# Kernel tuning notes

Hardware: AMD Instinct MI355X
Metric: run time of the kernel (lower is better)

Reference implementation:

```python
import jax, jax.numpy as jnp
import numpy as np

B, L, E, H = 4, 2048, 1024, 16
HD = E // H  # head_dim = 64


def setup_inputs() -> dict:
    key = jax.random.key(0)
    ks = jax.random.split(key, 10)
    s = 1.0 / np.sqrt(E)
    return {
        "x": jax.random.normal(ks[0], (B, L, E), dtype=jnp.float32),
        "mask": jax.random.randint(ks[1], (B, L), 0, 2, dtype=jnp.int32),
        "Wq": jax.random.normal(ks[2], (E, E), dtype=jnp.float32) * s,
        "bq": jnp.zeros((E,), dtype=jnp.float32),
        "Wk": jax.random.normal(ks[3], (E, E), dtype=jnp.float32) * s,
        "bk": jnp.zeros((E,), dtype=jnp.float32),
        "Wv": jax.random.normal(ks[4], (E, E), dtype=jnp.float32) * s,
        "bv": jnp.zeros((E,), dtype=jnp.float32),
        "Wo": jax.random.normal(ks[5], (E, E), dtype=jnp.float32) * s,
        "bo": jnp.zeros((E,), dtype=jnp.float32),
    }


def _separate_heads(t):
    # Faithful to the torch code: a raw reshape (B, L, E) -> (B, H, L, HD),
    # NOT the usual (B, L, H, HD) + transpose.
    return t.reshape(B, H, L, HD)


def reference(x, mask, Wq, bq, Wk, bk, Wv, bv, Wo, bo):
    q = _separate_heads(x @ Wq.T + bq)
    k = _separate_heads(x @ Wk.T + bk)
    v = _separate_heads(x @ Wv.T + bv)
    scores = jnp.einsum('bhqd,bhkd->bhqk', q, k) / np.sqrt(HD).astype(np.float32)
    m = mask[:, None, None, :]  # (B,1,1,L) broadcast over (B,H,L,L)
    scores = jnp.where(m == 0, jnp.float32(-1e10), scores)
    attn = jax.nn.softmax(scores, axis=-1)
    out = jnp.einsum('bhqk,bhkd->bhqd', attn, v)
    out = out.transpose(0, 2, 1, 3).reshape(B, L, E)
    return out @ Wo.T + bo
```

## Files before the change

kernel.cpp:

```cpp
#include <hip/hip_runtime.h>
#include <hip/hip_bf16.h>

namespace {
constexpr int kB = 4, kL = 2048, kE = 1024, kH = 16, kHD = 64;
constexpr float kCs = 0.18033688f;
}

typedef __attribute__((ext_vector_type(8))) short bf16x8;
typedef __attribute__((ext_vector_type(4))) float f32x4;

__device__ __forceinline__ short f2bf(float f) {
  __hip_bfloat16 h = __float2bfloat16(f);
  return *reinterpret_cast<short*>(&h);
}

__device__ __forceinline__ void load_lds16(const void* g, void* l) {
  __builtin_amdgcn_global_load_lds((const __attribute__((address_space(1))) void*)g,
                                   (__attribute__((address_space(3))) void*)l, 16, 0, 0);
}
__device__ __forceinline__ void load_lds4(const void* g, void* l) {
  __builtin_amdgcn_global_load_lds((const __attribute__((address_space(1))) void*)g,
                                   (__attribute__((address_space(3))) void*)l, 4, 0, 0);
}

__global__ __launch_bounds__(256) void k_prep(const float* __restrict__ x,
                                              const float* __restrict__ w0,
                                              const float* __restrict__ w1,
                                              const float* __restrict__ w2,
                                              const float* __restrict__ w3,
                                              const int* __restrict__ mask,
                                              short* __restrict__ xb,
                                              short* __restrict__ wdst,
                                              float* __restrict__ mkf) {
  const int bx = blockIdx.x;
  const int tid = threadIdx.x;
  if (bx < 8192) {
    int i = (bx * 256 + tid) * 4;
    float4 v = *reinterpret_cast<const float4*>(x + i);
    short4 o;
    o.x = f2bf(v.x); o.y = f2bf(v.y); o.z = f2bf(v.z); o.w = f2bf(v.w);
    *reinterpret_cast<short4*>(xb + i) = o;
  } else if (bx < 12288) {
    int b2 = bx - 8192;
    int seg = b2 >> 10;
    const float* s = seg == 0 ? w0 : seg == 1 ? w1 : seg == 2 ? w2 : w3;
    int local = ((b2 & 1023) * 256 + tid) * 4;
    float4 v = *reinterpret_cast<const float4*>(s + local);
    short4 o;
    o.x = f2bf(v.x); o.y = f2bf(v.y); o.z = f2bf(v.z); o.w = f2bf(v.w);
    *reinterpret_cast<short4*>(wdst + seg * 1048576 + local) = o;
  } else {
    int i = (bx - 12288) * 256 + tid;
    mkf[i] = mask[i] != 0 ? -10.0f : -1.0e10f;
  }
}

__global__ __launch_bounds__(256) void k_trv(const short* __restrict__ Vl,
                                             short* __restrict__ Vt) {
  __shared__ unsigned T[64 * 33];
  const int t = threadIdx.x;
  const int hb = blockIdx.y;
  const int l0 = blockIdx.x * 64;
  const short* src = Vl + hb * 131072;
  short* dst = Vt + hb * 131072;
  const int d8 = (t & 7) * 8;
  const int lp = t >> 3;
  const uint4 va = *reinterpret_cast<const uint4*>(src + (l0 + 2 * lp) * 64 + d8);
  const uint4 vb = *reinterpret_cast<const uint4*>(src + (l0 + 2 * lp + 1) * 64 + d8);
  const unsigned a[4] = {va.x, va.y, va.z, va.w};
  const unsigned b[4] = {vb.x, vb.y, vb.z, vb.w};
#pragma unroll
  for (int j = 0; j < 4; ++j) {
    unsigned z0 = __builtin_amdgcn_perm(b[j], a[j], 0x05040100u);
    unsigned z1 = __builtin_amdgcn_perm(b[j], a[j], 0x07060302u);
    T[(d8 + 2 * j) * 33 + lp] = z0;
    T[(d8 + 2 * j + 1) * 33 + lp] = z1;
  }
  __syncthreads();
  const int u = (t & 7) * 4;
#pragma unroll
  for (int h2 = 0; h2 < 2; ++h2) {
    int d = (t >> 3) + h2 * 32;
    uint4 r;
    r.x = T[d * 33 + u];     r.y = T[d * 33 + u + 1];
    r.z = T[d * 33 + u + 2]; r.w = T[d * 33 + u + 3];
    *reinterpret_cast<uint4*>(dst + d * 2048 + l0 + u * 2) = r;
  }
}

struct GemmCore256 {
  f32x4 acc[4][4];
  int tid, w, lane, quad, m16, wm, wn;
  __device__ __forceinline__ void run(const short* __restrict__ A,
                                      const short* __restrict__ W,
                                      int bm0, int bn0, short* S) {
    tid = threadIdx.x;
    w = tid >> 6; lane = tid & 63; quad = lane >> 4; m16 = lane & 15;
    wm = (w >> 1) * 64; wn = (w & 1) * 64;
#pragma unroll
    for (int i = 0; i < 4; ++i)
#pragma unroll
      for (int j = 0; j < 4; ++j) acc[i][j] = (f32x4){0, 0, 0, 0};

    const int srow = tid >> 3;
    const int sunit = (tid & 7) ^ (srow & 7);
    const short* Ag = A + (bm0 + srow) * 1024 + sunit * 8;
    const short* Wg = W + (bn0 + srow) * 1024 + sunit * 8;
    const int x7 = m16 & 7;
    const int u0 = (quad ^ x7) * 8;
    const int u1 = u0 ^ 32;
    const int baseA = (wm + m16) * 64;
    const int baseB = 16384 + (wn + m16) * 64;

#define STG_A(Sb, T, c) load_lds16(Ag + (c) * 65536 + (T) * 64, (Sb) + (c) * 4096 + tid * 8)
#define STG_B(Sb, T, c) load_lds16(Wg + (c) * 65536 + (T) * 64, (Sb) + 16384 + (c) * 4096 + tid * 8)

    short* S1 = S + 24576;
    STG_A(S, 0, 0); STG_A(S, 0, 1); STG_A(S, 0, 2); STG_A(S, 0, 3);
    STG_B(S, 0, 0); STG_B(S, 0, 1);
    STG_A(S1, 1, 0); STG_A(S1, 1, 1); STG_A(S1, 1, 2); STG_A(S1, 1, 3);
    STG_B(S1, 1, 0); STG_B(S1, 1, 1);
    asm volatile("s_waitcnt vmcnt(6)" ::: "memory");
    __builtin_amdgcn_s_barrier();
    __builtin_amdgcn_sched_barrier(0);

    int bc = 0;
    for (int t = 0; t < 16; ++t) {
      short* Sc = S + bc * 24576;
      int b2 = bc + 2; if (b2 >= 3) b2 -= 3;
      short* Sp = S + b2 * 24576;
      const bool pf = (t < 14);

      bf16x8 a[4][2], b[4][2];
#pragma unroll
      for (int i = 0; i < 4; ++i) {
        a[i][0] = *reinterpret_cast<const bf16x8*>(&Sc[baseA + i * 1024 + u0]);
        a[i][1] = *reinterpret_cast<const bf16x8*>(&Sc[baseA + i * 1024 + u1]);
      }
#pragma unroll
      for (int j = 0; j < 4; ++j) {
        b[j][0] = *reinterpret_cast<const bf16x8*>(&Sc[baseB + j * 1024 + u0]);
        b[j][1] = *reinterpret_cast<const bf16x8*>(&Sc[baseB + j * 1024 + u1]);
      }
      if (pf) {
        STG_A(Sp, t + 2, 0); STG_A(Sp, t + 2, 1); STG_A(Sp, t + 2, 2); STG_A(Sp, t + 2, 3);
        STG_B(Sp, t + 2, 0); STG_B(Sp, t + 2, 1);
      }
      __builtin_amdgcn_s_setprio(1);
#pragma unroll
      for (int i = 0; i < 4; ++i)
#pragma unroll
        for (int j = 0; j < 4; ++j) {
          acc[i][j] = __builtin_amdgcn_mfma_f32_16x16x32_bf16(a[i][0], b[j][0], acc[i][j], 0, 0, 0);
          acc[i][j] = __builtin_amdgcn_mfma_f32_16x16x32_bf16(a[i][1], b[j][1], acc[i][j], 0, 0, 0);
        }
      __builtin_amdgcn_s_setprio(0);
      if (pf) { asm volatile("s_waitcnt vmcnt(6)" ::: "memory"); }
      else    { asm volatile("s_waitcnt vmcnt(0)" ::: "memory"); }
      __builtin_amdgcn_s_barrier();
      __builtin_amdgcn_sched_barrier(0);
      bc += 1; if (bc >= 3) bc -= 3;
    }
#undef STG_A
#undef STG_B
  }
};

__global__ __launch_bounds__(512, 2) void k_gemm_qkv(const short* __restrict__ xb,
                                                     const short* __restrict__ Wq,
                                                     const short* __restrict__ Wk,
                                                     const short* __restrict__ Wv,
                                                     const float* __restrict__ bq,
                                                     const float* __restrict__ bk,
                                                     const float* __restrict__ bv,
                                                     short* __restrict__ Q,
                                                     short* __restrict__ K,
                                                     short* __restrict__ Vl) {
  __shared__ __attribute__((aligned(16))) short S[73728];
  const int l = blockIdx.x + 24 * blockIdx.y;
  const int xcd = l & 7, wv_ = l >> 3;
  const int bm0 = (xcd + 8 * (wv_ & 3)) * 256;
  const int colsel = wv_ >> 2;
  const int sel = colsel >> 3;
  const int bn0 = (colsel & 7) * 128;
  const short* W = sel == 0 ? Wq : sel == 1 ? Wk : Wv;
  const float* bias = sel == 0 ? bq : sel == 1 ? bk : bv;

  GemmCore256 g;
  g.run(xb, W, bm0, bn0, S);

  float bj[4];
#pragma unroll
  for (int j = 0; j < 4; ++j) bj[j] = bias[bn0 + g.wn + j * 16 + g.m16];

  short* C = sel == 0 ? Q : sel == 1 ? K : Vl;
  float sc = sel == 0 ? kCs : 1.0f;
#pragma unroll
  for (int i = 0; i < 4; ++i)
#pragma unroll
    for (int j = 0; j < 4; ++j)
#pragma unroll
      for (int rg = 0; rg < 4; ++rg) {
        int row = bm0 + g.wm + i * 16 + g.quad * 4 + rg;
        int col = bn0 + g.wn + j * 16 + g.m16;
        C[row * 1024 + col] = f2bf((g.acc[i][j][rg] + bj[j]) * sc);
      }
}

__global__ __launch_bounds__(512, 2) void k_gemm_out(const short* __restrict__ A,
                                                     const short* __restrict__ Wo,
                                                     const float* __restrict__ bo,
                                                     float* __restrict__ C) {
  __shared__ __attribute__((aligned(16))) short S[73728];
  const int l = blockIdx.x + 8 * blockIdx.y;
  const int xcd = l & 7, wv_ = l >> 3;
  const int bm0 = (xcd + 8 * (wv_ & 3)) * 256;
  const int bn0 = (wv_ >> 2) * 128;
  GemmCore256 g;
  g.run(A, Wo, bm0, bn0, S);
  float bj[4];
#pragma unroll
  for (int j = 0; j < 4; ++j) bj[j] = bo[bn0 + g.wn + j * 16 + g.m16];
#pragma unroll
  for (int i = 0; i < 4; ++i)
#pragma unroll
    for (int j = 0; j < 4; ++j)
#pragma unroll
      for (int rg = 0; rg < 4; ++rg) {
        int row = bm0 + g.wm + i * 16 + g.quad * 4 + rg;
        int col = bn0 + g.wn + j * 16 + g.m16;
        C[row * 1024 + col] = g.acc[i][j][rg] + bj[j];
      }
}

__global__ __launch_bounds__(512, 4) void k_attn(const short* __restrict__ Q,
                                                 const short* __restrict__ Km,
                                                 const short* __restrict__ Vt,
                                                 const float* __restrict__ Mg,
                                                 short* __restrict__ Out) {
  __shared__ __attribute__((aligned(16))) short U[16896];
  __shared__ __attribute__((aligned(16))) short Ks[4096];
  __shared__ __attribute__((aligned(16))) short Vs[4096];
  __shared__ __attribute__((aligned(16))) float Mk[64];

  const int tid = threadIdx.x;
  const int w = tid >> 6, lane = tid & 63;
  const int quad = lane >> 4, m16 = lane & 15;
  const int lid = blockIdx.x + 8 * blockIdx.y;
  const int xcd = lid & 7, wv_ = lid >> 3;
  const int hb = xcd + 8 * (wv_ & 7);
  const int qb = wv_ >> 3;
  const int b = hb >> 4, h = hb & 15;
  const int wb = w * 2112;

  const short* Qh = Q + hb * (kL * kHD) + qb * 256 * kHD;
  const short* Kh = Km + hb * (kL * kHD);
  const short* Vh = Vt + hb * (kL * kHD);
  const float* Mb = Mg + b * kL;

  const int srow = tid >> 3;
  const int sunit = (tid & 7) ^ (srow & 7);
  const int x7 = m16 & 7;
  const int u0 = (quad ^ x7) * 8;
  const int u1 = u0 ^ 32;

#pragma unroll
  for (int c = 0; c < 4; ++c)
    load_lds16(Qh + (c * 64 + srow) * 64 + sunit * 8, &U[c * 4096 + tid * 8]);
  __syncthreads();
  bf16x8 qf[2][2];
#pragma unroll
  for (int i = 0; i < 2; ++i) {
    qf[i][0] = *reinterpret_cast<const bf16x8*>(&U[(w * 32 + i * 16 + m16) * 64 + u0]);
    qf[i][1] = *reinterpret_cast<const bf16x8*>(&U[(w * 32 + i * 16 + m16) * 64 + u1]);
  }

  bf16x8 ones;
#pragma unroll
  for (int e = 0; e < 8; ++e) ones[e] = (short)0x3F80;

  f32x4 oacc[2][4] = {};
  f32x4 lacc[2] = {};

  for (int kb = 0; kb < 32; ++kb) {
    int kbase = kb * 64;
    load_lds16(Kh + (kbase + srow) * 64 + sunit * 8, &Ks[tid * 8]);
    load_lds16(Vh + srow * 2048 + kbase + sunit * 8, &Vs[tid * 8]);
    if (tid < 64) load_lds4(Mb + kbase + tid, &Mk[tid]);
    __syncthreads();

    f32x4 ST[4][2];
    __builtin_amdgcn_s_setprio(1);
#pragma unroll
    for (int j = 0; j < 4; ++j) {
      float4 mj4 = *reinterpret_cast<const float4*>(&Mk[j * 16 + quad * 4]);
      f32x4 init; init[0] = mj4.x; init[1] = mj4.y; init[2] = mj4.z; init[3] = mj4.w;
#pragma unroll
      for (int i = 0; i < 2; ++i) ST[j][i] = init;
      bf16x8 kf0 = *reinterpret_cast<const bf16x8*>(&Ks[(j * 16 + m16) * 64 + u0]);
      bf16x8 kf1 = *reinterpret_cast<const bf16x8*>(&Ks[(j * 16 + m16) * 64 + u1]);
#pragma unroll
      for (int i = 0; i < 2; ++i) {
        ST[j][i] = __builtin_amdgcn_mfma_f32_16x16x32_bf16(kf0, qf[i][0], ST[j][i], 0, 0, 0);
        ST[j][i] = __builtin_amdgcn_mfma_f32_16x16x32_bf16(kf1, qf[i][1], ST[j][i], 0, 0, 0);
      }
    }
    __builtin_amdgcn_s_setprio(0);

    const int kc_w = (quad >> 1);
    const int inner = (quad & 1) * 4;
#pragma unroll
    for (int j = 0; j < 4; ++j)
#pragma unroll
      for (int i = 0; i < 2; ++i) {
        float p0 = __builtin_amdgcn_exp2f(ST[j][i][0]);
        float p1 = __builtin_amdgcn_exp2f(ST[j][i][1]);
        float p2 = __builtin_amdgcn_exp2f(ST[j][i][2]);
        float p3 = __builtin_amdgcn_exp2f(ST[j][i][3]);
        uint2 pk;
        pk.x = __builtin_amdgcn_perm(__builtin_bit_cast(unsigned, p1),
                                     __builtin_bit_cast(unsigned, p0), 0x07060302u);
        pk.y = __builtin_amdgcn_perm(__builtin_bit_cast(unsigned, p3),
                                     __builtin_bit_cast(unsigned, p2), 0x07060302u);
        *reinterpret_cast<uint2*>(
            &U[wb + (j * 2 + kc_w) * 264 + (i * 16 + m16) * 8 + inner]) = pk;
      }
    asm volatile("s_waitcnt lgkmcnt(0)" ::: "memory");

    bf16x8 pf[2][2];
#pragma unroll
    for (int i = 0; i < 2; ++i)
#pragma unroll
      for (int s = 0; s < 2; ++s)
        pf[i][s] = *reinterpret_cast<const bf16x8*>(
            &U[wb + (s * 4 + quad) * 264 + (i * 16 + m16) * 8]);

    __builtin_amdgcn_s_setprio(1);
#pragma unroll
    for (int i = 0; i < 2; ++i) {
      lacc[i] = __builtin_amdgcn_mfma_f32_16x16x32_bf16(pf[i][0], ones, lacc[i], 0, 0, 0);
      lacc[i] = __builtin_amdgcn_mfma_f32_16x16x32_bf16(pf[i][1], ones, lacc[i], 0, 0, 0);
    }

#pragma unroll
    for (int j = 0; j < 4; ++j) {
      bf16x8 vf0 = *reinterpret_cast<const bf16x8*>(&Vs[(j * 16 + m16) * 64 + u0]);
      bf16x8 vf1 = *reinterpret_cast<const bf16x8*>(&Vs[(j * 16 + m16) * 64 + u1]);
#pragma unroll
      for (int i = 0; i < 2; ++i) {
        oacc[i][j] = __builtin_amdgcn_mfma_f32_16x16x32_bf16(pf[i][0], vf0, oacc[i][j], 0, 0, 0);
        oacc[i][j] = __builtin_amdgcn_mfma_f32_16x16x32_bf16(pf[i][1], vf1, oacc[i][j], 0, 0, 0);
      }
    }
    __builtin_amdgcn_s_setprio(0);
    __syncthreads();
  }

#pragma unroll
  for (int i = 0; i < 2; ++i)
#pragma unroll
    for (int j = 0; j < 4; ++j) {
      int d = j * 16 + m16;
#pragma unroll
      for (int rg = 0; rg < 4; ++rg) {
        int ql = qb * 256 + w * 32 + i * 16 + quad * 4 + rg;
        Out[(b * kL + ql) * kE + h * kHD + d] =
            f2bf(oacc[i][j][rg] / lacc[i][rg]);
      }
    }
}

extern "C" void kernel_launch(void* const* d_in, const int* in_sizes, int n_in,
                              void* d_out, int out_size, void* d_ws, size_t ws_size,
                              hipStream_t stream) {
  const float* x  = (const float*)d_in[0];
  const int* mask = (const int*)d_in[1];
  const float* Wq = (const float*)d_in[2];
  const float* bq = (const float*)d_in[3];
  const float* Wk = (const float*)d_in[4];
  const float* bk = (const float*)d_in[5];
  const float* Wv = (const float*)d_in[6];
  const float* bv = (const float*)d_in[7];
  const float* Wo = (const float*)d_in[8];
  const float* bo = (const float*)d_in[9];

  short* ws  = (short*)d_ws;
  short* xb  = ws;
  short* Wqb = xb  + 8388608;
  short* Wkb = Wqb + 1048576;
  short* Wvb = Wkb + 1048576;
  short* Wob = Wvb + 1048576;
  short* Qb  = Wob + 1048576;
  short* Kb  = Qb  + 8388608;
  short* Vtb = Kb  + 8388608;
  short* AOb = Vtb + 8388608;
  float* Mkf = (float*)(AOb + 8388608);

  k_prep<<<12320, 256, 0, stream>>>(x, Wq, Wk, Wv, Wo, mask, xb, Wqb, Mkf);
  k_gemm_qkv<<<dim3(24, 32), 512, 0, stream>>>(xb, Wqb, Wkb, Wvb, bq, bk, bv, Qb, Kb, AOb);
  k_trv<<<dim3(32, 64), 256, 0, stream>>>(AOb, Vtb);
  k_attn<<<dim3(8, 64), 512, 0, stream>>>(Qb, Kb, Vtb, Mkf, AOb);
  k_gemm_out<<<dim3(8, 32), 512, 0, stream>>>(AOb, Wob, bo, (float*)d_out);
}
```

Baseline: 258.1 us.

## Split GEMM K-step into four ping-pong phases interleaving LDS reads, prefetch, and MFMA

Each K-iteration of the projection GEMM mainloop is split into four quadrant phases. Each phase loads only the A/B fragments it needs from LDS, issues part of the global-to-LDS prefetch, and runs a 2x2 block of MFMAs, with barriers and setprio between phases. The aim is to overlap LDS reads and global loads with matrix math across the two co-resident waves in a ping-pong schedule. The extra barriers per iteration add synchronization cost and can stall if the waves do not interleave as intended.

```diff
diff --git a/kernel.cpp b/kernel.cpp
--- a/kernel.cpp
+++ b/kernel.cpp
@@ -114,6 +114,7 @@
 
 #define STG_A(Sb, T, c) load_lds16(Ag + (c) * 65536 + (T) * 64, (Sb) + (c) * 4096 + tid * 8)
 #define STG_B(Sb, T, c) load_lds16(Wg + (c) * 65536 + (T) * 64, (Sb) + 16384 + (c) * 4096 + tid * 8)
+#define MFMA_(d, x, y) d = __builtin_amdgcn_mfma_f32_16x16x32_bf16(x, y, d, 0, 0, 0)
 
     short* S1 = S + 24576;
     STG_A(S, 0, 0); STG_A(S, 0, 1); STG_A(S, 0, 2); STG_A(S, 0, 3);
@@ -132,27 +133,80 @@
       const bool pf = (t < 14);
 
       bf16x8 a[4][2], b[4][2];
-#pragma unroll
-      for (int i = 0; i < 4; ++i) {
+
+#pragma unroll
+      for (int i = 0; i < 2; ++i) {
         a[i][0] = *reinterpret_cast<const bf16x8*>(&Sc[baseA + i * 1024 + u0]);
         a[i][1] = *reinterpret_cast<const bf16x8*>(&Sc[baseA + i * 1024 + u1]);
-      }
-#pragma unroll
-      for (int j = 0; j < 4; ++j) {
+        b[i][0] = *reinterpret_cast<const bf16x8*>(&Sc[baseB + i * 1024 + u0]);
+        b[i][1] = *reinterpret_cast<const bf16x8*>(&Sc[baseB + i * 1024 + u1]);
+      }
+      if (pf) { STG_A(Sp, t + 2, 0); STG_A(Sp, t + 2, 1); }
+      __builtin_amdgcn_s_barrier();
+      asm volatile("s_waitcnt lgkmcnt(0)" ::: "memory");
+      __builtin_amdgcn_sched_barrier(0);
+      __builtin_amdgcn_s_setprio(1);
+#pragma unroll
+      for (int i = 0; i < 2; ++i)
+#pragma unroll
+        for (int j = 0; j < 2; ++j) {
+          MFMA_(acc[i][j], a[i][0], b[j][0]);
+          MFMA_(acc[i][j], a[i][1], b[j][1]);
+        }
+      __builtin_amdgcn_s_setprio(0);
+      __builtin_amdgcn_s_barrier();
+      __builtin_amdgcn_sched_barrier(0);
+
+#pragma unroll
+      for (int j = 2; j < 4; ++j) {
         b[j][0] = *reinterpret_cast<const bf16x8*>(&Sc[baseB + j * 1024 + u0]);
         b[j][1] = *reinterpret_cast<const bf16x8*>(&Sc[baseB + j * 1024 + u1]);
       }
-      if (pf) {
-        STG_A(Sp, t + 2, 0); STG_A(Sp, t + 2, 1); STG_A(Sp, t + 2, 2); STG_A(Sp, t + 2, 3);
-        STG_B(Sp, t + 2, 0); STG_B(Sp, t + 2, 1);
-      }
+      if (pf) { STG_A(Sp, t + 2, 2); STG_A(Sp, t + 2, 3); }
+      __builtin_amdgcn_s_barrier();
+      asm volatile("s_waitcnt lgkmcnt(0)" ::: "memory");
+      __builtin_amdgcn_sched_barrier(0);
       __builtin_amdgcn_s_setprio(1);
 #pragma unroll
-      for (int i = 0; i < 4; ++i)
-#pragma unroll
-        for (int j = 0; j < 4; ++j) {
-          acc[i][j] = __builtin_amdgcn_mfma_f32_16x16x32_bf16(a[i][0], b[j][0], acc[i][j], 0, 0, 0);
-          acc[i][j] = __builtin_amdgcn_mfma_f32_16x16x32_bf16(a[i][1], b[j][1], acc[i][j], 0, 0, 0);
+      for (int i = 0; i < 2; ++i)
+#pragma unroll
+        for (int j = 2; j < 4; ++j) {
+          MFMA_(acc[i][j], a[i][0], b[j][0]);
+          MFMA_(acc[i][j], a[i][1], b[j][1]);
+        }
+      __builtin_amdgcn_s_setprio(0);
+      __builtin_amdgcn_s_barrier();
+      __builtin_amdgcn_sched_barrier(0);
+
+#pragma unroll
+      for (int i = 2; i < 4; ++i) {
+        a[i][0] = *reinterpret_cast<const bf16x8*>(&Sc[baseA + i * 1024 + u0]);
+        a[i][1] = *reinterpret_cast<const bf16x8*>(&Sc[baseA + i * 1024 + u1]);
+      }
+      if (pf) { STG_B(Sp, t + 2, 0); }
+      __builtin_amdgcn_s_barrier();
+      asm volatile("s_waitcnt lgkmcnt(0)" ::: "memory");
+      __builtin_amdgcn_sched_barrier(0);
+      __builtin_amdgcn_s_setprio(1);
+#pragma unroll
+      for (int i = 2; i < 4; ++i)
+#pragma unroll
+        for (int j = 0; j < 2; ++j) {
+          MFMA_(acc[i][j], a[i][0], b[j][0]);
+          MFMA_(acc[i][j], a[i][1], b[j][1]);
+        }
+      __builtin_amdgcn_s_setprio(0);
+      __builtin_amdgcn_s_barrier();
+      __builtin_amdgcn_sched_barrier(0);
+
+      if (pf) { STG_B(Sp, t + 2, 1); }
+      __builtin_amdgcn_s_setprio(1);
+#pragma unroll
+      for (int i = 2; i < 4; ++i)
+#pragma unroll
+        for (int j = 2; j < 4; ++j) {
+          MFMA_(acc[i][j], a[i][0], b[j][0]);
+          MFMA_(acc[i][j], a[i][1], b[j][1]);
         }
       __builtin_amdgcn_s_setprio(0);
       if (pf) { asm volatile("s_waitcnt vmcnt(6)" ::: "memory"); }
@@ -163,6 +217,7 @@
     }
 #undef STG_A
 #undef STG_B
+#undef MFMA_
   }
 };
 
```

New measurement: 264.6 us. 1.03x slower.
